# Performance work log

Hardware: AMD Instinct MI355X
Metric: run time of the kernel (lower is better)

Reference implementation:

```python
import jax, jax.numpy as jnp
import numpy as np

H = 25  # fixed state size per module source
N_STEPS = 10


def _lstm_cell(x, h, c, W_ih, W_hh, b_ih, b_hh):
    # PyTorch LSTMCell: gates ordered i, f, g, o
    gates = x @ W_ih.T + b_ih + h @ W_hh.T + b_hh  # [B, 4H]
    i, f, g, o = jnp.split(gates, 4, axis=-1)
    c_new = jax.nn.sigmoid(f) * c + jax.nn.sigmoid(i) * jnp.tanh(g)
    h_new = jax.nn.sigmoid(o) * jnp.tanh(c_new)
    return h_new, c_new


def setup_inputs() -> dict:
    key = jax.random.key(0)
    ks = jax.random.split(key, 11)
    B, A = 131072, 18

    def u(k, shape, fan_in, fan_out):
        bound = np.sqrt(6.0 / (fan_in + fan_out)).astype(np.float32)
        return jax.random.uniform(k, shape, jnp.float32, -bound, bound)

    state = jax.random.normal(ks[0], (B, H), jnp.float32)
    # LSTMCell weights [4H, H]; biases zeroed per module init
    W_ih_enc = u(ks[1], (4 * H, H), H, 4 * H)
    W_hh_enc = u(ks[2], (4 * H, H), H, 4 * H)
    b_ih_enc = jnp.zeros((4 * H,), jnp.float32)
    b_hh_enc = jnp.zeros((4 * H,), jnp.float32)
    W_ih_dec = u(ks[3], (4 * H, H), H, 4 * H)
    W_hh_dec = u(ks[4], (4 * H, H), H, 4 * H)
    b_ih_dec = jnp.zeros((4 * H,), jnp.float32)
    b_hh_dec = jnp.zeros((4 * H,), jnp.float32)
    # actor head: norm_col_init std=0.01, bias 0
    w = jax.random.normal(ks[5], (A, H), jnp.float32)
    W_act = w * (0.01 / jnp.sqrt((w ** 2).sum(1, keepdims=True)))
    b_act = jnp.zeros((A,), jnp.float32)
    return {
        "state_repr_input": state,
        "W_ih_enc": W_ih_enc, "W_hh_enc": W_hh_enc, "b_ih_enc": b_ih_enc, "b_hh_enc": b_hh_enc,
        "W_ih_dec": W_ih_dec, "W_hh_dec": W_hh_dec, "b_ih_dec": b_ih_dec, "b_hh_dec": b_hh_dec,
        "W_act": W_act, "b_act": b_act,
    }


def reference(state_repr_input, W_ih_enc, W_hh_enc, b_ih_enc, b_hh_enc,
              W_ih_dec, W_hh_dec, b_ih_dec, b_hh_dec, W_act, b_act):
    B = state_repr_input.shape[0]
    zeros = jnp.zeros_like(state_repr_input)

    # Encoder: input to each step is previous hx (first step: state)
    def enc_step(carry, _):
        inp, h, c = carry
        h, c = _lstm_cell(inp, h, c, W_ih_enc, W_hh_enc, b_ih_enc, b_hh_enc)
        return (h, h, c), h

    (_, _, _), enc_hs = jax.lax.scan(enc_step, (state_repr_input, zeros, zeros), None, length=N_STEPS)
    # enc_hs: [10, B, 25]

    # Decoder: consumes encoder outputs in order
    def dec_step(carry, x):
        h, c = carry
        h, c = _lstm_cell(x, h, c, W_ih_dec, W_hh_dec, b_ih_dec, b_hh_dec)
        return (h, c), None

    (hx_dec, _), _ = jax.lax.scan(dec_step, (zeros, zeros), enc_hs)

    actor_lang = hx_dec @ W_act.T + b_act  # [B, A]
    return actor_lang, enc_hs
```

## Files before the change

### kernel.cpp

```cpp
#include <hip/hip_runtime.h>


#define HH 25
#define NSTEP 10
#define AOUT 18
#define WPB 4
#define BLK (WPB * 64)
#define NFRG 26
#define FPAD 40
#define LOG2E 1.44269504088896340736f

typedef __attribute__((ext_vector_type(8))) short short8;
typedef __attribute__((ext_vector_type(4))) float f32x4;

__device__ __forceinline__ short f2bf(float x) {
    unsigned u = __float_as_uint(x);
    u += 0x7fffu + ((u >> 16) & 1u);
    return (short)(u >> 16);
}
__device__ __forceinline__ unsigned cvtpk(float lo, float hi) {
    unsigned r;
    asm("v_cvt_pk_bf16_f32 %0, %1, %2" : "=v"(r) : "v"(lo), "v"(hi));
    return r;
}
#if __has_builtin(__builtin_amdgcn_exp2f)
#define EXP2(x) __builtin_amdgcn_exp2f(x)
#else
#define EXP2(x) exp2f(x)
#endif
#define RCP(x) __builtin_amdgcn_rcpf(x)
#define MFMA16(a, b, c) __builtin_amdgcn_mfma_f32_16x16x32_bf16((a), (b), (c), 0, 0, 0)

#define ACT_ELEM(A0, A1, A2, A3, CREF, HOUT)                                   \
    {                                                                          \
        float Ei = EXP2(A0);                                                   \
        float Ef = EXP2(A1);                                                   \
        float Eg = EXP2(A2);                                                   \
        float Eo = EXP2(A3);                                                   \
        float Pf = 1.f + Ef;                                                   \
        float Pig = (1.f + Ei) * (1.f + Eg);                                   \
        float c = fmaf(CREF, Pig, (Eg - 1.f) * Pf) * RCP(Pf * Pig);            \
        CREF = c;                                                              \
        float Ec = EXP2(2.f * LOG2E * c);                                      \
        float Pc = 1.f + Ec;                                                   \
        HOUT = (Pc - 2.f) * RCP(Pc * (1.f + Eo));                              \
    }

__global__ __launch_bounds__(BLK, 4)
void langnn_mfma16(const float* __restrict__ state,
                   const float* __restrict__ Wih_e, const float* __restrict__ Whh_e,
                   const float* __restrict__ bih_e, const float* __restrict__ bhh_e,
                   const float* __restrict__ Wih_d, const float* __restrict__ Whh_d,
                   const float* __restrict__ bih_d, const float* __restrict__ bhh_d,
                   const float* __restrict__ Wact, const float* __restrict__ bact,
                   float* __restrict__ out, int B)
{
    __shared__ __align__(16) short sFrag[NFRG][64][8];
    __shared__ __align__(16) short sH[2][WPB][16][FPAD];

    const int tid  = threadIdx.x;
    const int lane = tid & 63;
    const int w    = tid >> 6;
    const int r    = lane & 15;
    const int g    = lane >> 4;

    for (int i = tid; i < NFRG * 64; i += BLK) {
        const int idx = i >> 6, l = i & 63;
        const int lj = l & 15, lg = l >> 4;
        const float *W1 = nullptr, *W2 = nullptr, *B1 = nullptr, *B2 = nullptr;
        int gt = 0, jt, jmax = HH;
        if (idx < 8)       { gt = idx >> 1;        jt = idx & 1; W1 = Wih_e; W2 = Whh_e; B1 = bih_e; B2 = bhh_e; }
        else if (idx < 16) { gt = (idx - 8) >> 1;  jt = idx & 1; W1 = Wih_d; B1 = bih_d; B2 = bhh_d; }
        else if (idx < 24) { gt = (idx - 16) >> 1; jt = idx & 1; W1 = Whh_d; }
        else               { jt = idx - 24;        W1 = Wact;    B1 = bact;  jmax = AOUT; }
        const bool actor = (idx >= 24);
        const float sc = actor ? 1.f : (gt == 2 ? 2.f * LOG2E : -LOG2E);
        const int col = jt * 16 + lj;
        const int nrow = actor ? col : gt * HH + col;
        for (int e = 0; e < 8; ++e) {
            const int k = lg * 8 + e;
            float v = 0.f;
            if (col < jmax) {
                if (k < HH) {
                    v = W1[nrow * HH + k];
                    if (W2) v += W2[nrow * HH + k];
                    v *= sc;
                } else if (k == HH && B1) {
                    v = B1[nrow];
                    if (B2) v += B2[nrow];
                    v *= sc;
                }
            }
            sFrag[idx][l][e] = f2bf(v);
        }
    }
    {
        int* z = (int*)sH;
        for (int i = tid; i < 2 * WPB * 16 * (FPAD / 2); i += BLK)
            z[i] = ((i % (FPAD / 2)) == 12) ? 0x3F800000 : 0;
    }
    __syncthreads();

    const int b0 = (blockIdx.x * WPB + w) * 16;
    float* pe = out + (size_t)B * AOUT + (size_t)(b0 + g * 4) * HH + r;

    float ce[2][4], cd[2][4];
    #pragma unroll
    for (int jt = 0; jt < 2; ++jt)
        #pragma unroll
        for (int q = 0; q < 4; ++q) { ce[jt][q] = 0.f; cd[jt][q] = 0.f; }

    short8 aE, aD;
    {
        const float* sp0 = state + (size_t)(b0 + r) * HH;
        #pragma unroll
        for (int e = 0; e < 8; ++e) {
            const int k = g * 8 + e;
            aE[e] = (k < HH) ? f2bf(sp0[k]) : (k == HH ? (short)0x3F80 : (short)0);
            aD[e] = (k == HH) ? (short)0x3F80 : (short)0;
        }
    }

    {
        short8 W0f[8];
        #pragma unroll
        for (int gt = 0; gt < 4; ++gt) {
            const float sc = (gt == 2 ? 2.f * LOG2E : -LOG2E);
            #pragma unroll
            for (int jt = 0; jt < 2; ++jt) {
                const int col = jt * 16 + r;
                short8 v8;
                #pragma unroll
                for (int e = 0; e < 8; ++e) {
                    const int k = g * 8 + e;
                    float v = 0.f;
                    if (col < HH) {
                        if (k < HH)       v = Wih_e[(gt * HH + col) * HH + k] * sc;
                        else if (k == HH) v = (bih_e[gt * HH + col] + bhh_e[gt * HH + col]) * sc;
                    }
                    v8[e] = f2bf(v);
                }
                W0f[gt * 2 + jt] = v8;
            }
        }
        #pragma unroll
        for (int jt = 0; jt < 2; ++jt) {
            f32x4 acc[4];
            #pragma unroll
            for (int gt = 0; gt < 4; ++gt) {
                f32x4 z; z[0] = z[1] = z[2] = z[3] = 0.f;
                acc[gt] = MFMA16(aE, W0f[gt * 2 + jt], z);
            }
            float hv[4];
            #pragma unroll
            for (int q = 0; q < 4; ++q)
                ACT_ELEM(acc[0][q], acc[1][q], acc[2][q], acc[3][q], ce[jt][q], hv[q]);
            if (jt == 0 || r < 9) {
                float* p = pe + jt * 16;
                p[0] = hv[0]; p[HH] = hv[1]; p[2 * HH] = hv[2]; p[3 * HH] = hv[3];
                unsigned p01 = cvtpk(hv[0], hv[1]), p23 = cvtpk(hv[2], hv[3]);
                short* sp = &sH[0][w][g * 4][jt * 16 + r];
                sp[0]        = (short)p01;
                sp[FPAD]     = (short)(p01 >> 16);
                sp[2 * FPAD] = (short)p23;
                sp[3 * FPAD] = (short)(p23 >> 16);
            }
        }
        aE = *(const short8*)&sH[0][w][r][g * 8];
        pe += (size_t)B * HH;
    }

    #pragma unroll 1
    for (int t = 0; t < NSTEP - 1; ++t) {
        #pragma unroll
        for (int jt = 0; jt < 2; ++jt) {
            f32x4 accD[4], accE[4];
            #pragma unroll
            for (int gt = 0; gt < 4; ++gt) {
                short8 Bx = *(const short8*)&sFrag[8 + gt * 2 + jt][lane][0];
                short8 Bh = *(const short8*)&sFrag[16 + gt * 2 + jt][lane][0];
                short8 Be = *(const short8*)&sFrag[gt * 2 + jt][lane][0];
                f32x4 z; z[0] = z[1] = z[2] = z[3] = 0.f;
                accD[gt] = MFMA16(aD, Bh, MFMA16(aE, Bx, z));
                accE[gt] = MFMA16(aE, Be, z);
            }
            float hvD[4], hvE[4];
            #pragma unroll
            for (int q = 0; q < 4; ++q) {
                ACT_ELEM(accD[0][q], accD[1][q], accD[2][q], accD[3][q], cd[jt][q], hvD[q]);
                ACT_ELEM(accE[0][q], accE[1][q], accE[2][q], accE[3][q], ce[jt][q], hvE[q]);
            }
            if (jt == 0 || r < 9) {
                float* p = pe + jt * 16;
                p[0] = hvE[0]; p[HH] = hvE[1]; p[2 * HH] = hvE[2]; p[3 * HH] = hvE[3];
                unsigned d01 = cvtpk(hvD[0], hvD[1]), d23 = cvtpk(hvD[2], hvD[3]);
                unsigned e01 = cvtpk(hvE[0], hvE[1]), e23 = cvtpk(hvE[2], hvE[3]);
                short* spD = &sH[1][w][g * 4][jt * 16 + r];
                short* spE = &sH[0][w][g * 4][jt * 16 + r];
                spD[0]        = (short)d01;
                spD[FPAD]     = (short)(d01 >> 16);
                spD[2 * FPAD] = (short)d23;
                spD[3 * FPAD] = (short)(d23 >> 16);
                spE[0]        = (short)e01;
                spE[FPAD]     = (short)(e01 >> 16);
                spE[2 * FPAD] = (short)e23;
                spE[3 * FPAD] = (short)(e23 >> 16);
            }
        }
        aE = *(const short8*)&sH[0][w][r][g * 8];
        aD = *(const short8*)&sH[1][w][r][g * 8];
        pe += (size_t)B * HH;
    }

    #pragma unroll
    for (int jt = 0; jt < 2; ++jt) {
        f32x4 acc[4];
        #pragma unroll
        for (int gt = 0; gt < 4; ++gt) {
            short8 Bx = *(const short8*)&sFrag[8 + gt * 2 + jt][lane][0];
            short8 Bh = *(const short8*)&sFrag[16 + gt * 2 + jt][lane][0];
            f32x4 z; z[0] = z[1] = z[2] = z[3] = 0.f;
            acc[gt] = MFMA16(aD, Bh, MFMA16(aE, Bx, z));
        }
        float hv[4];
        #pragma unroll
        for (int q = 0; q < 4; ++q)
            ACT_ELEM(acc[0][q], acc[1][q], acc[2][q], acc[3][q], cd[jt][q], hv[q]);
        if (jt == 0 || r < 9) {
            unsigned p01 = cvtpk(hv[0], hv[1]), p23 = cvtpk(hv[2], hv[3]);
            short* sp = &sH[1][w][g * 4][jt * 16 + r];
            sp[0]        = (short)p01;
            sp[FPAD]     = (short)(p01 >> 16);
            sp[2 * FPAD] = (short)p23;
            sp[3 * FPAD] = (short)(p23 >> 16);
        }
    }
    aD = *(const short8*)&sH[1][w][r][g * 8];

    #pragma unroll
    for (int jt = 0; jt < 2; ++jt) {
        short8 Bf = *(const short8*)&sFrag[24 + jt][lane][0];
        f32x4 z; z[0] = z[1] = z[2] = z[3] = 0.f;
        f32x4 o = MFMA16(aD, Bf, z);
        if (jt == 0 || r < 2) {
            float* p = out + (size_t)(b0 + g * 4) * AOUT + jt * 16 + r;
            p[0] = o[0]; p[AOUT] = o[1]; p[2 * AOUT] = o[2]; p[3 * AOUT] = o[3];
        }
    }
}

extern "C" void kernel_launch(void* const* d_in, const int* in_sizes, int n_in,
                              void* d_out, int out_size, void* d_ws, size_t ws_size,
                              hipStream_t stream) {
    const float* state = (const float*)d_in[0];
    const float* Wih_e = (const float*)d_in[1];
    const float* Whh_e = (const float*)d_in[2];
    const float* bih_e = (const float*)d_in[3];
    const float* bhh_e = (const float*)d_in[4];
    const float* Wih_d = (const float*)d_in[5];
    const float* Whh_d = (const float*)d_in[6];
    const float* bih_d = (const float*)d_in[7];
    const float* bhh_d = (const float*)d_in[8];
    const float* Wact  = (const float*)d_in[9];
    const float* bact  = (const float*)d_in[10];

    int B = in_sizes[0] / HH;
    int grid = B / (WPB * 16);

    hipLaunchKernelGGL(langnn_mfma16, dim3(grid), dim3(BLK), 0, stream,
                       state, Wih_e, Whh_e, bih_e, bhh_e,
                       Wih_d, Whh_d, bih_d, bhh_d, Wact, bact,
                       (float*)d_out, B);
}
```

Baseline: 115.1 us.

## Swap MFMA operands so hidden state stays in registers, dropping LDS round-trip

Result: faster. 110.1 us (-4.4%).

```diff
diff --git a/kernel.cpp b/kernel.cpp
--- a/kernel.cpp
+++ b/kernel.cpp
@@ -7,11 +7,11 @@
 #define WPB 4
 #define BLK (WPB * 64)
 #define NFRG 26
-#define FPAD 40
 #define LOG2E 1.44269504088896340736f
 
 typedef __attribute__((ext_vector_type(8))) short short8;
 typedef __attribute__((ext_vector_type(4))) float f32x4;
+typedef __attribute__((ext_vector_type(4))) unsigned u32x4;
 
 __device__ __forceinline__ short f2bf(float x) {
     unsigned u = __float_as_uint(x);
@@ -19,9 +19,9 @@
     return (short)(u >> 16);
 }
 __device__ __forceinline__ unsigned cvtpk(float lo, float hi) {
-    unsigned r;
-    asm("v_cvt_pk_bf16_f32 %0, %1, %2" : "=v"(r) : "v"(lo), "v"(hi));
-    return r;
+    unsigned rr;
+    asm("v_cvt_pk_bf16_f32 %0, %1, %2" : "=v"(rr) : "v"(lo), "v"(hi));
+    return rr;
 }
 #if __has_builtin(__builtin_amdgcn_exp2f)
 #define EXP2(x) __builtin_amdgcn_exp2f(x)
@@ -47,16 +47,15 @@
     }
 
 __global__ __launch_bounds__(BLK, 4)
-void langnn_mfma16(const float* __restrict__ state,
-                   const float* __restrict__ Wih_e, const float* __restrict__ Whh_e,
-                   const float* __restrict__ bih_e, const float* __restrict__ bhh_e,
-                   const float* __restrict__ Wih_d, const float* __restrict__ Whh_d,
-                   const float* __restrict__ bih_d, const float* __restrict__ bhh_d,
-                   const float* __restrict__ Wact, const float* __restrict__ bact,
-                   float* __restrict__ out, int B)
+void langnn_swap(const float* __restrict__ state,
+                 const float* __restrict__ Wih_e, const float* __restrict__ Whh_e,
+                 const float* __restrict__ bih_e, const float* __restrict__ bhh_e,
+                 const float* __restrict__ Wih_d, const float* __restrict__ Whh_d,
+                 const float* __restrict__ bih_d, const float* __restrict__ bhh_d,
+                 const float* __restrict__ Wact, const float* __restrict__ bact,
+                 float* __restrict__ out, int B)
 {
     __shared__ __align__(16) short sFrag[NFRG][64][8];
-    __shared__ __align__(16) short sH[2][WPB][16][FPAD];
 
     const int tid  = threadIdx.x;
     const int lane = tid & 63;
@@ -68,24 +67,24 @@
         const int idx = i >> 6, l = i & 63;
         const int lj = l & 15, lg = l >> 4;
         const float *W1 = nullptr, *W2 = nullptr, *B1 = nullptr, *B2 = nullptr;
-        int gt = 0, jt, jmax = HH;
-        if (idx < 8)       { gt = idx >> 1;        jt = idx & 1; W1 = Wih_e; W2 = Whh_e; B1 = bih_e; B2 = bhh_e; }
-        else if (idx < 16) { gt = (idx - 8) >> 1;  jt = idx & 1; W1 = Wih_d; B1 = bih_d; B2 = bhh_d; }
-        else if (idx < 24) { gt = (idx - 16) >> 1; jt = idx & 1; W1 = Whh_d; }
-        else               { jt = idx - 24;        W1 = Wact;    B1 = bact;  jmax = AOUT; }
+        int gt = 0, hf, rmax = HH;
+        if (idx < 8)       { gt = idx >> 1;        hf = idx & 1; W1 = Wih_e; W2 = Whh_e; B1 = bih_e; B2 = bhh_e; }
+        else if (idx < 16) { gt = (idx - 8) >> 1;  hf = idx & 1; W1 = Wih_d; B1 = bih_d; B2 = bhh_d; }
+        else if (idx < 24) { gt = (idx - 16) >> 1; hf = idx & 1; W1 = Whh_d; }
+        else               { hf = idx - 24;        W1 = Wact;    B1 = bact;  rmax = AOUT; }
         const bool actor = (idx >= 24);
         const float sc = actor ? 1.f : (gt == 2 ? 2.f * LOG2E : -LOG2E);
-        const int col = jt * 16 + lj;
-        const int nrow = actor ? col : gt * HH + col;
+        const int row  = hf * 16 + lj;
+        const int nrow = actor ? row : gt * HH + row;
         for (int e = 0; e < 8; ++e) {
-            const int k = lg * 8 + e;
+            const int k = (e < 4) ? lg * 4 + e : 16 + lg * 4 + (e - 4);
             float v = 0.f;
-            if (col < jmax) {
+            if (row < rmax) {
                 if (k < HH) {
                     v = W1[nrow * HH + k];
                     if (W2) v += W2[nrow * HH + k];
                     v *= sc;
-                } else if (k == HH && B1) {
+                } else if (k == 31 && B1) {
                     v = B1[nrow];
                     if (B2) v += B2[nrow];
                     v *= sc;
@@ -94,158 +93,126 @@
             sFrag[idx][l][e] = f2bf(v);
         }
     }
-    {
-        int* z = (int*)sH;
-        for (int i = tid; i < 2 * WPB * 16 * (FPAD / 2); i += BLK)
-            z[i] = ((i % (FPAD / 2)) == 12) ? 0x3F800000 : 0;
-    }
     __syncthreads();
 
     const int b0 = (blockIdx.x * WPB + w) * 16;
-    float* pe = out + (size_t)B * AOUT + (size_t)(b0 + g * 4) * HH + r;
+    float* encBase = out + (size_t)B * AOUT + (size_t)(b0 + r) * HH;
 
     float ce[2][4], cd[2][4];
     #pragma unroll
-    for (int jt = 0; jt < 2; ++jt)
-        #pragma unroll
-        for (int q = 0; q < 4; ++q) { ce[jt][q] = 0.f; cd[jt][q] = 0.f; }
-
-    short8 aE, aD;
+    for (int hf = 0; hf < 2; ++hf)
+        #pragma unroll
+        for (int q = 0; q < 4; ++q) { ce[hf][q] = 0.f; cd[hf][q] = 0.f; }
+
+    short8 hE, hD;
     {
-        const float* sp0 = state + (size_t)(b0 + r) * HH;
+        const float* sp = state + (size_t)(b0 + r) * HH;
         #pragma unroll
         for (int e = 0; e < 8; ++e) {
-            const int k = g * 8 + e;
-            aE[e] = (k < HH) ? f2bf(sp0[k]) : (k == HH ? (short)0x3F80 : (short)0);
-            aD[e] = (k == HH) ? (short)0x3F80 : (short)0;
-        }
-    }
-
-    {
-        short8 W0f[8];
-        #pragma unroll
-        for (int gt = 0; gt < 4; ++gt) {
-            const float sc = (gt == 2 ? 2.f * LOG2E : -LOG2E);
-            #pragma unroll
-            for (int jt = 0; jt < 2; ++jt) {
-                const int col = jt * 16 + r;
-                short8 v8;
-                #pragma unroll
-                for (int e = 0; e < 8; ++e) {
-                    const int k = g * 8 + e;
-                    float v = 0.f;
-                    if (col < HH) {
-                        if (k < HH)       v = Wih_e[(gt * HH + col) * HH + k] * sc;
-                        else if (k == HH) v = (bih_e[gt * HH + col] + bhh_e[gt * HH + col]) * sc;
-                    }
-                    v8[e] = f2bf(v);
-                }
-                W0f[gt * 2 + jt] = v8;
-            }
-        }
-        #pragma unroll
-        for (int jt = 0; jt < 2; ++jt) {
-            f32x4 acc[4];
-            #pragma unroll
-            for (int gt = 0; gt < 4; ++gt) {
-                f32x4 z; z[0] = z[1] = z[2] = z[3] = 0.f;
-                acc[gt] = MFMA16(aE, W0f[gt * 2 + jt], z);
-            }
-            float hv[4];
+            const int k = (e < 4) ? g * 4 + e : 16 + g * 4 + (e - 4);
+            hE[e] = (k < HH) ? f2bf(sp[k]) : (k == 31 ? (short)0x3F80 : (short)0);
+            hD[e] = (k == 31) ? (short)0x3F80 : (short)0;
+        }
+    }
+
+    auto actCell = [&](f32x4 (&acc)[8], float (&cc)[2][4], float (&hv)[2][4]) {
+        #pragma unroll
+        for (int hf = 0; hf < 2; ++hf)
             #pragma unroll
             for (int q = 0; q < 4; ++q)
-                ACT_ELEM(acc[0][q], acc[1][q], acc[2][q], acc[3][q], ce[jt][q], hv[q]);
-            if (jt == 0 || r < 9) {
-                float* p = pe + jt * 16;
-                p[0] = hv[0]; p[HH] = hv[1]; p[2 * HH] = hv[2]; p[3 * HH] = hv[3];
-                unsigned p01 = cvtpk(hv[0], hv[1]), p23 = cvtpk(hv[2], hv[3]);
-                short* sp = &sH[0][w][g * 4][jt * 16 + r];
-                sp[0]        = (short)p01;
-                sp[FPAD]     = (short)(p01 >> 16);
-                sp[2 * FPAD] = (short)p23;
-                sp[3 * FPAD] = (short)(p23 >> 16);
+                ACT_ELEM(acc[0 + hf][q], acc[2 + hf][q], acc[4 + hf][q], acc[6 + hf][q],
+                         cc[hf][q], hv[hf][q]);
+    };
+    auto packH = [&](float (&hv)[2][4]) -> short8 {
+        union { u32x4 d; short8 s; } u;
+        u.d[0] = cvtpk(hv[0][0], hv[0][1]);
+        u.d[1] = cvtpk(hv[0][2], hv[0][3]);
+        u.d[2] = cvtpk(hv[1][0], hv[1][1]);
+        u.d[3] = cvtpk(hv[1][2], (g == 3) ? 1.0f : hv[1][3]);
+        return u.s;
+    };
+    auto storeEnc = [&](int t, float (&hv)[2][4]) {
+        float* p = encBase + (size_t)t * B * HH;
+        #pragma unroll
+        for (int q = 0; q < 4; ++q) p[g * 4 + q] = hv[0][q];
+        #pragma unroll
+        for (int q = 0; q < 4; ++q)
+            if (g * 4 + q < 9) p[16 + g * 4 + q] = hv[1][q];
+    };
+
+    {
+        f32x4 acc[8];
+        #pragma unroll
+        for (int idx = 0; idx < 8; ++idx) {
+            const int gt = idx >> 1, hf = idx & 1;
+            const float sc = (gt == 2) ? 2.f * LOG2E : -LOG2E;
+            const int row = hf * 16 + r;
+            short8 Wf;
+            #pragma unroll
+            for (int e = 0; e < 8; ++e) {
+                const int k = (e < 4) ? g * 4 + e : 16 + g * 4 + (e - 4);
+                float v = 0.f;
+                if (row < HH) {
+                    if (k < HH)       v = Wih_e[(gt * HH + row) * HH + k] * sc;
+                    else if (k == 31) v = (bih_e[gt * HH + row] + bhh_e[gt * HH + row]) * sc;
+                }
+                Wf[e] = f2bf(v);
             }
-        }
-        aE = *(const short8*)&sH[0][w][r][g * 8];
-        pe += (size_t)B * HH;
-    }
+            f32x4 z; z[0] = z[1] = z[2] = z[3] = 0.f;
+            acc[idx] = MFMA16(Wf, hE, z);
+        }
+        float hv[2][4];
+        actCell(acc, ce, hv);
+        storeEnc(0, hv);
+        hE = packH(hv);
+    }
+
+    auto decCell = [&]() {
+        f32x4 acc[8];
+        #pragma unroll
+        for (int idx = 0; idx < 8; ++idx) {
+            short8 Wx = *(const short8*)&sFrag[8 + idx][lane][0];
+            short8 Wh = *(const short8*)&sFrag[16 + idx][lane][0];
+            f32x4 z; z[0] = z[1] = z[2] = z[3] = 0.f;
+            acc[idx] = MFMA16(Wh, hD, MFMA16(Wx, hE, z));
+        }
+        float hv[2][4];
+        actCell(acc, cd, hv);
+        hD = packH(hv);
+    };
+    auto encCell = [&](int t) {
+        f32x4 acc[8];
+        #pragma unroll
+        for (int idx = 0; idx < 8; ++idx) {
+            short8 Wf = *(const short8*)&sFrag[idx][lane][0];
+            f32x4 z; z[0] = z[1] = z[2] = z[3] = 0.f;
+            acc[idx] = MFMA16(Wf, hE, z);
+        }
+        float hv[2][4];
+        actCell(acc, ce, hv);
+        storeEnc(t, hv);
+        hE = packH(hv);
+    };
 
     #pragma unroll 1
     for (int t = 0; t < NSTEP - 1; ++t) {
-        #pragma unroll
-        for (int jt = 0; jt < 2; ++jt) {
-            f32x4 accD[4], accE[4];
-            #pragma unroll
-            for (int gt = 0; gt < 4; ++gt) {
-                short8 Bx = *(const short8*)&sFrag[8 + gt * 2 + jt][lane][0];
-                short8 Bh = *(const short8*)&sFrag[16 + gt * 2 + jt][lane][0];
-                short8 Be = *(const short8*)&sFrag[gt * 2 + jt][lane][0];
-                f32x4 z; z[0] = z[1] = z[2] = z[3] = 0.f;
-                accD[gt] = MFMA16(aD, Bh, MFMA16(aE, Bx, z));
-                accE[gt] = MFMA16(aE, Be, z);
-            }
-            float hvD[4], hvE[4];
-            #pragma unroll
-            for (int q = 0; q < 4; ++q) {
-                ACT_ELEM(accD[0][q], accD[1][q], accD[2][q], accD[3][q], cd[jt][q], hvD[q]);
-                ACT_ELEM(accE[0][q], accE[1][q], accE[2][q], accE[3][q], ce[jt][q], hvE[q]);
-            }
-            if (jt == 0 || r < 9) {
-                float* p = pe + jt * 16;
-                p[0] = hvE[0]; p[HH] = hvE[1]; p[2 * HH] = hvE[2]; p[3 * HH] = hvE[3];
-                unsigned d01 = cvtpk(hvD[0], hvD[1]), d23 = cvtpk(hvD[2], hvD[3]);
-                unsigned e01 = cvtpk(hvE[0], hvE[1]), e23 = cvtpk(hvE[2], hvE[3]);
-                short* spD = &sH[1][w][g * 4][jt * 16 + r];
-                short* spE = &sH[0][w][g * 4][jt * 16 + r];
-                spD[0]        = (short)d01;
-                spD[FPAD]     = (short)(d01 >> 16);
-                spD[2 * FPAD] = (short)d23;
-                spD[3 * FPAD] = (short)(d23 >> 16);
-                spE[0]        = (short)e01;
-                spE[FPAD]     = (short)(e01 >> 16);
-                spE[2 * FPAD] = (short)e23;
-                spE[3 * FPAD] = (short)(e23 >> 16);
-            }
-        }
-        aE = *(const short8*)&sH[0][w][r][g * 8];
-        aD = *(const short8*)&sH[1][w][r][g * 8];
-        pe += (size_t)B * HH;
-    }
-
-    #pragma unroll
-    for (int jt = 0; jt < 2; ++jt) {
-        f32x4 acc[4];
-        #pragma unroll
-        for (int gt = 0; gt < 4; ++gt) {
-            short8 Bx = *(const short8*)&sFrag[8 + gt * 2 + jt][lane][0];
-            short8 Bh = *(const short8*)&sFrag[16 + gt * 2 + jt][lane][0];
-            f32x4 z; z[0] = z[1] = z[2] = z[3] = 0.f;
-            acc[gt] = MFMA16(aD, Bh, MFMA16(aE, Bx, z));
-        }
-        float hv[4];
+        decCell();
+        encCell(t + 1);
+    }
+    decCell();
+
+    {
+        short8 W0 = *(const short8*)&sFrag[24][lane][0];
+        short8 W1 = *(const short8*)&sFrag[25][lane][0];
+        f32x4 z; z[0] = z[1] = z[2] = z[3] = 0.f;
+        f32x4 a0 = MFMA16(W0, hD, z);
+        f32x4 a1 = MFMA16(W1, hD, z);
+        float* p = out + (size_t)(b0 + r) * AOUT;
+        #pragma unroll
+        for (int q = 0; q < 4; ++q) p[g * 4 + q] = a0[q];
         #pragma unroll
         for (int q = 0; q < 4; ++q)
-            ACT_ELEM(acc[0][q], acc[1][q], acc[2][q], acc[3][q], cd[jt][q], hv[q]);
-        if (jt == 0 || r < 9) {
-            unsigned p01 = cvtpk(hv[0], hv[1]), p23 = cvtpk(hv[2], hv[3]);
-            short* sp = &sH[1][w][g * 4][jt * 16 + r];
-            sp[0]        = (short)p01;
-            sp[FPAD]     = (short)(p01 >> 16);
-            sp[2 * FPAD] = (short)p23;
-            sp[3 * FPAD] = (short)(p23 >> 16);
-        }
-    }
-    aD = *(const short8*)&sH[1][w][r][g * 8];
-
-    #pragma unroll
-    for (int jt = 0; jt < 2; ++jt) {
-        short8 Bf = *(const short8*)&sFrag[24 + jt][lane][0];
-        f32x4 z; z[0] = z[1] = z[2] = z[3] = 0.f;
-        f32x4 o = MFMA16(aD, Bf, z);
-        if (jt == 0 || r < 2) {
-            float* p = out + (size_t)(b0 + g * 4) * AOUT + jt * 16 + r;
-            p[0] = o[0]; p[AOUT] = o[1]; p[2 * AOUT] = o[2]; p[3 * AOUT] = o[3];
-        }
+            if (16 + g * 4 + q < AOUT) p[16 + g * 4 + q] = a1[q];
     }
 }
 
@@ -267,7 +234,7 @@
     int B = in_sizes[0] / HH;
     int grid = B / (WPB * 16);
 
-    hipLaunchKernelGGL(langnn_mfma16, dim3(grid), dim3(BLK), 0, stream,
+    hipLaunchKernelGGL(langnn_swap, dim3(grid), dim3(BLK), 0, stream,
                        state, Wih_e, Whh_e, bih_e, bhh_e,
                        Wih_d, Whh_d, bih_d, bhh_d, Wact, bact,
                        (float*)d_out, B);
```

## Warp-specialize encoder and decoder waves with block barriers and two M-tiles

Applied to the files above, without the earlier changes.

New measurement: 107.0 us. 7.0% less time.

```diff
diff --git a/kernel.cpp b/kernel.cpp
--- a/kernel.cpp
+++ b/kernel.cpp
@@ -4,10 +4,11 @@
 #define HH 25
 #define NSTEP 10
 #define AOUT 18
-#define WPB 4
-#define BLK (WPB * 64)
-#define NFRG 26
-#define FPAD 40
+#define BLK 512
+#define NWENC 4
+#define MT 2
+#define NFRG 24
+#define FPAD 32
 #define LOG2E 1.44269504088896340736f
 
 typedef __attribute__((ext_vector_type(8))) short short8;
@@ -19,9 +20,9 @@
     return (short)(u >> 16);
 }
 __device__ __forceinline__ unsigned cvtpk(float lo, float hi) {
-    unsigned r;
-    asm("v_cvt_pk_bf16_f32 %0, %1, %2" : "=v"(r) : "v"(lo), "v"(hi));
-    return r;
+    unsigned rr;
+    asm("v_cvt_pk_bf16_f32 %0, %1, %2" : "=v"(rr) : "v"(lo), "v"(hi));
+    return rr;
 }
 #if __has_builtin(__builtin_amdgcn_exp2f)
 #define EXP2(x) __builtin_amdgcn_exp2f(x)
@@ -47,16 +48,17 @@
     }
 
 __global__ __launch_bounds__(BLK, 4)
-void langnn_mfma16(const float* __restrict__ state,
-                   const float* __restrict__ Wih_e, const float* __restrict__ Whh_e,
-                   const float* __restrict__ bih_e, const float* __restrict__ bhh_e,
-                   const float* __restrict__ Wih_d, const float* __restrict__ Whh_d,
-                   const float* __restrict__ bih_d, const float* __restrict__ bhh_d,
-                   const float* __restrict__ Wact, const float* __restrict__ bact,
-                   float* __restrict__ out, int B)
+void langnn_ws(const float* __restrict__ state,
+               const float* __restrict__ Wih_e, const float* __restrict__ Whh_e,
+               const float* __restrict__ bih_e, const float* __restrict__ bhh_e,
+               const float* __restrict__ Wih_d, const float* __restrict__ Whh_d,
+               const float* __restrict__ bih_d, const float* __restrict__ bhh_d,
+               const float* __restrict__ Wact, const float* __restrict__ bact,
+               float* __restrict__ out, int B)
 {
     __shared__ __align__(16) short sFrag[NFRG][64][8];
-    __shared__ __align__(16) short sH[2][WPB][16][FPAD];
+    __shared__ __align__(16) short sHE[2][128][FPAD];
+    __shared__ __align__(16) short sHD[NWENC][32][FPAD];
 
     const int tid  = threadIdx.x;
     const int lane = tid & 63;
@@ -68,19 +70,17 @@
         const int idx = i >> 6, l = i & 63;
         const int lj = l & 15, lg = l >> 4;
         const float *W1 = nullptr, *W2 = nullptr, *B1 = nullptr, *B2 = nullptr;
-        int gt = 0, jt, jmax = HH;
+        int gt, jt;
         if (idx < 8)       { gt = idx >> 1;        jt = idx & 1; W1 = Wih_e; W2 = Whh_e; B1 = bih_e; B2 = bhh_e; }
         else if (idx < 16) { gt = (idx - 8) >> 1;  jt = idx & 1; W1 = Wih_d; B1 = bih_d; B2 = bhh_d; }
-        else if (idx < 24) { gt = (idx - 16) >> 1; jt = idx & 1; W1 = Whh_d; }
-        else               { jt = idx - 24;        W1 = Wact;    B1 = bact;  jmax = AOUT; }
-        const bool actor = (idx >= 24);
-        const float sc = actor ? 1.f : (gt == 2 ? 2.f * LOG2E : -LOG2E);
+        else               { gt = (idx - 16) >> 1; jt = idx & 1; W1 = Whh_d; }
+        const float sc = (gt == 2 ? 2.f * LOG2E : -LOG2E);
         const int col = jt * 16 + lj;
-        const int nrow = actor ? col : gt * HH + col;
+        const int nrow = gt * HH + col;
         for (int e = 0; e < 8; ++e) {
             const int k = lg * 8 + e;
             float v = 0.f;
-            if (col < jmax) {
+            if (col < HH) {
                 if (k < HH) {
                     v = W1[nrow * HH + k];
                     if (W2) v += W2[nrow * HH + k];
@@ -95,41 +95,58 @@
         }
     }
     {
-        int* z = (int*)sH;
-        for (int i = tid; i < 2 * WPB * 16 * (FPAD / 2); i += BLK)
-            z[i] = ((i % (FPAD / 2)) == 12) ? 0x3F800000 : 0;
+        int* zE = (int*)sHE;
+        for (int i = tid; i < 2 * 128 * (FPAD / 2); i += BLK)
+            zE[i] = ((i % (FPAD / 2)) == 12) ? 0x3F800000 : 0;
+        int* zD = (int*)sHD;
+        for (int i = tid; i < NWENC * 32 * (FPAD / 2); i += BLK)
+            zD[i] = ((i % (FPAD / 2)) == 12) ? 0x3F800000 : 0;
     }
     __syncthreads();
 
-    const int b0 = (blockIdx.x * WPB + w) * 16;
-    float* pe = out + (size_t)B * AOUT + (size_t)(b0 + g * 4) * HH + r;
-
-    float ce[2][4], cd[2][4];
+    const bool isEnc = (w < NWENC);
+    const int wl = isEnc ? w : (w - NWENC);
+    const int rowBase = wl * 32;
+    const int gBase = blockIdx.x * 128 + rowBase;
+
+    float cc[MT][2][4];
     #pragma unroll
-    for (int jt = 0; jt < 2; ++jt)
-        #pragma unroll
-        for (int q = 0; q < 4; ++q) { ce[jt][q] = 0.f; cd[jt][q] = 0.f; }
-
-    short8 aE, aD;
-    {
-        const float* sp0 = state + (size_t)(b0 + r) * HH;
+    for (int mt = 0; mt < MT; ++mt)
+        #pragma unroll
+        for (int jt = 0; jt < 2; ++jt)
+            #pragma unroll
+            for (int q = 0; q < 4; ++q) cc[mt][jt][q] = 0.f;
+
+    short8 aE[MT], aD[MT];
+    #pragma unroll
+    for (int mt = 0; mt < MT; ++mt) {
         #pragma unroll
         for (int e = 0; e < 8; ++e) {
             const int k = g * 8 + e;
-            aE[e] = (k < HH) ? f2bf(sp0[k]) : (k == HH ? (short)0x3F80 : (short)0);
-            aD[e] = (k == HH) ? (short)0x3F80 : (short)0;
-        }
-    }
-
-    {
-        short8 W0f[8];
-        #pragma unroll
-        for (int gt = 0; gt < 4; ++gt) {
-            const float sc = (gt == 2 ? 2.f * LOG2E : -LOG2E);
-            #pragma unroll
-            for (int jt = 0; jt < 2; ++jt) {
+            aD[mt][e] = (k == HH) ? (short)0x3F80 : (short)0;
+        }
+    }
+    if (isEnc) {
+        #pragma unroll
+        for (int mt = 0; mt < MT; ++mt) {
+            const float* sp0 = state + (size_t)(gBase + mt * 16 + r) * HH;
+            #pragma unroll
+            for (int e = 0; e < 8; ++e) {
+                const int k = g * 8 + e;
+                aE[mt][e] = (k < HH) ? f2bf(sp0[k]) : (k == HH ? (short)0x3F80 : (short)0);
+            }
+        }
+    }
+
+    if (isEnc) {
+        #pragma unroll
+        for (int jt = 0; jt < 2; ++jt) {
+            f32x4 acc[MT][4];
+            #pragma unroll
+            for (int gt = 0; gt < 4; ++gt) {
+                const float sc = (gt == 2) ? 2.f * LOG2E : -LOG2E;
                 const int col = jt * 16 + r;
-                short8 v8;
+                short8 Wf;
                 #pragma unroll
                 for (int e = 0; e < 8; ++e) {
                     const int k = g * 8 + e;
@@ -138,113 +155,178 @@
                         if (k < HH)       v = Wih_e[(gt * HH + col) * HH + k] * sc;
                         else if (k == HH) v = (bih_e[gt * HH + col] + bhh_e[gt * HH + col]) * sc;
                     }
-                    v8[e] = f2bf(v);
-                }
-                W0f[gt * 2 + jt] = v8;
-            }
-        }
+                    Wf[e] = f2bf(v);
+                }
+                f32x4 z; z[0] = z[1] = z[2] = z[3] = 0.f;
+                #pragma unroll
+                for (int mt = 0; mt < MT; ++mt) acc[mt][gt] = MFMA16(aE[mt], Wf, z);
+            }
+            #pragma unroll
+            for (int mt = 0; mt < MT; ++mt) {
+                float hv[4];
+                #pragma unroll
+                for (int q = 0; q < 4; ++q)
+                    ACT_ELEM(acc[mt][0][q], acc[mt][1][q], acc[mt][2][q], acc[mt][3][q],
+                             cc[mt][jt][q], hv[q]);
+                if (jt == 0 || r < 9) {
+                    float* p = out + (size_t)B * AOUT
+                             + (size_t)(gBase + mt * 16 + g * 4) * HH + jt * 16 + r;
+                    p[0] = hv[0]; p[HH] = hv[1]; p[2 * HH] = hv[2]; p[3 * HH] = hv[3];
+                    unsigned p01 = cvtpk(hv[0], hv[1]), p23 = cvtpk(hv[2], hv[3]);
+                    short* sp = &sHE[0][rowBase + mt * 16 + g * 4][jt * 16 + r];
+                    sp[0]        = (short)p01;
+                    sp[FPAD]     = (short)(p01 >> 16);
+                    sp[2 * FPAD] = (short)p23;
+                    sp[3 * FPAD] = (short)(p23 >> 16);
+                }
+            }
+        }
+        #pragma unroll
+        for (int mt = 0; mt < MT; ++mt)
+            aE[mt] = *(const short8*)&sHE[0][rowBase + mt * 16 + r][g * 8];
+    }
+    __syncthreads();
+
+    #pragma unroll 1
+    for (int t = 1; t < NSTEP; ++t) {
+        if (isEnc) {
+            const int buf = t & 1;
+            #pragma unroll
+            for (int jt = 0; jt < 2; ++jt) {
+                f32x4 acc[MT][4];
+                #pragma unroll
+                for (int gt = 0; gt < 4; ++gt) {
+                    short8 Bf = *(const short8*)&sFrag[gt * 2 + jt][lane][0];
+                    f32x4 z; z[0] = z[1] = z[2] = z[3] = 0.f;
+                    #pragma unroll
+                    for (int mt = 0; mt < MT; ++mt) acc[mt][gt] = MFMA16(aE[mt], Bf, z);
+                }
+                #pragma unroll
+                for (int mt = 0; mt < MT; ++mt) {
+                    float hv[4];
+                    #pragma unroll
+                    for (int q = 0; q < 4; ++q)
+                        ACT_ELEM(acc[mt][0][q], acc[mt][1][q], acc[mt][2][q], acc[mt][3][q],
+                                 cc[mt][jt][q], hv[q]);
+                    if (jt == 0 || r < 9) {
+                        float* p = out + (size_t)B * AOUT + (size_t)t * B * HH
+                                 + (size_t)(gBase + mt * 16 + g * 4) * HH + jt * 16 + r;
+                        p[0] = hv[0]; p[HH] = hv[1]; p[2 * HH] = hv[2]; p[3 * HH] = hv[3];
+                        unsigned p01 = cvtpk(hv[0], hv[1]), p23 = cvtpk(hv[2], hv[3]);
+                        short* sp = &sHE[buf][rowBase + mt * 16 + g * 4][jt * 16 + r];
+                        sp[0]        = (short)p01;
+                        sp[FPAD]     = (short)(p01 >> 16);
+                        sp[2 * FPAD] = (short)p23;
+                        sp[3 * FPAD] = (short)(p23 >> 16);
+                    }
+                }
+            }
+            #pragma unroll
+            for (int mt = 0; mt < MT; ++mt)
+                aE[mt] = *(const short8*)&sHE[buf][rowBase + mt * 16 + r][g * 8];
+        } else {
+            const int buf = (t - 1) & 1;
+            short8 aEd[MT];
+            #pragma unroll
+            for (int mt = 0; mt < MT; ++mt)
+                aEd[mt] = *(const short8*)&sHE[buf][rowBase + mt * 16 + r][g * 8];
+            #pragma unroll
+            for (int jt = 0; jt < 2; ++jt) {
+                f32x4 acc[MT][4];
+                #pragma unroll
+                for (int gt = 0; gt < 4; ++gt) {
+                    short8 Bx = *(const short8*)&sFrag[8 + gt * 2 + jt][lane][0];
+                    short8 Bh = *(const short8*)&sFrag[16 + gt * 2 + jt][lane][0];
+                    f32x4 z; z[0] = z[1] = z[2] = z[3] = 0.f;
+                    #pragma unroll
+                    for (int mt = 0; mt < MT; ++mt)
+                        acc[mt][gt] = MFMA16(aD[mt], Bh, MFMA16(aEd[mt], Bx, z));
+                }
+                #pragma unroll
+                for (int mt = 0; mt < MT; ++mt) {
+                    float hv[4];
+                    #pragma unroll
+                    for (int q = 0; q < 4; ++q)
+                        ACT_ELEM(acc[mt][0][q], acc[mt][1][q], acc[mt][2][q], acc[mt][3][q],
+                                 cc[mt][jt][q], hv[q]);
+                    if (jt == 0 || r < 9) {
+                        unsigned p01 = cvtpk(hv[0], hv[1]), p23 = cvtpk(hv[2], hv[3]);
+                        short* sp = &sHD[wl][mt * 16 + g * 4][jt * 16 + r];
+                        sp[0]        = (short)p01;
+                        sp[FPAD]     = (short)(p01 >> 16);
+                        sp[2 * FPAD] = (short)p23;
+                        sp[3 * FPAD] = (short)(p23 >> 16);
+                    }
+                }
+            }
+            #pragma unroll
+            for (int mt = 0; mt < MT; ++mt)
+                aD[mt] = *(const short8*)&sHD[wl][mt * 16 + r][g * 8];
+        }
+        __syncthreads();
+    }
+
+    if (!isEnc) {
+        short8 aEd[MT];
+        #pragma unroll
+        for (int mt = 0; mt < MT; ++mt)
+            aEd[mt] = *(const short8*)&sHE[(NSTEP - 1) & 1][rowBase + mt * 16 + r][g * 8];
         #pragma unroll
         for (int jt = 0; jt < 2; ++jt) {
-            f32x4 acc[4];
-            #pragma unroll
-            for (int gt = 0; gt < 4; ++gt) {
-                f32x4 z; z[0] = z[1] = z[2] = z[3] = 0.f;
-                acc[gt] = MFMA16(aE, W0f[gt * 2 + jt], z);
-            }
-            float hv[4];
-            #pragma unroll
-            for (int q = 0; q < 4; ++q)
-                ACT_ELEM(acc[0][q], acc[1][q], acc[2][q], acc[3][q], ce[jt][q], hv[q]);
-            if (jt == 0 || r < 9) {
-                float* p = pe + jt * 16;
-                p[0] = hv[0]; p[HH] = hv[1]; p[2 * HH] = hv[2]; p[3 * HH] = hv[3];
-                unsigned p01 = cvtpk(hv[0], hv[1]), p23 = cvtpk(hv[2], hv[3]);
-                short* sp = &sH[0][w][g * 4][jt * 16 + r];
-                sp[0]        = (short)p01;
-                sp[FPAD]     = (short)(p01 >> 16);
-                sp[2 * FPAD] = (short)p23;
-                sp[3 * FPAD] = (short)(p23 >> 16);
-            }
-        }
-        aE = *(const short8*)&sH[0][w][r][g * 8];
-        pe += (size_t)B * HH;
-    }
-
-    #pragma unroll 1
-    for (int t = 0; t < NSTEP - 1; ++t) {
-        #pragma unroll
-        for (int jt = 0; jt < 2; ++jt) {
-            f32x4 accD[4], accE[4];
+            f32x4 acc[MT][4];
             #pragma unroll
             for (int gt = 0; gt < 4; ++gt) {
                 short8 Bx = *(const short8*)&sFrag[8 + gt * 2 + jt][lane][0];
                 short8 Bh = *(const short8*)&sFrag[16 + gt * 2 + jt][lane][0];
-                short8 Be = *(const short8*)&sFrag[gt * 2 + jt][lane][0];
                 f32x4 z; z[0] = z[1] = z[2] = z[3] = 0.f;
-                accD[gt] = MFMA16(aD, Bh, MFMA16(aE, Bx, z));
-                accE[gt] = MFMA16(aE, Be, z);
-            }
-            float hvD[4], hvE[4];
-            #pragma unroll
-            for (int q = 0; q < 4; ++q) {
-                ACT_ELEM(accD[0][q], accD[1][q], accD[2][q], accD[3][q], cd[jt][q], hvD[q]);
-                ACT_ELEM(accE[0][q], accE[1][q], accE[2][q], accE[3][q], ce[jt][q], hvE[q]);
-            }
-            if (jt == 0 || r < 9) {
-                float* p = pe + jt * 16;
-                p[0] = hvE[0]; p[HH] = hvE[1]; p[2 * HH] = hvE[2]; p[3 * HH] = hvE[3];
-                unsigned d01 = cvtpk(hvD[0], hvD[1]), d23 = cvtpk(hvD[2], hvD[3]);
-                unsigned e01 = cvtpk(hvE[0], hvE[1]), e23 = cvtpk(hvE[2], hvE[3]);
-                short* spD = &sH[1][w][g * 4][jt * 16 + r];
-                short* spE = &sH[0][w][g * 4][jt * 16 + r];
-                spD[0]        = (short)d01;
-                spD[FPAD]     = (short)(d01 >> 16);
-                spD[2 * FPAD] = (short)d23;
-                spD[3 * FPAD] = (short)(d23 >> 16);
-                spE[0]        = (short)e01;
-                spE[FPAD]     = (short)(e01 >> 16);
-                spE[2 * FPAD] = (short)e23;
-                spE[3 * FPAD] = (short)(e23 >> 16);
-            }
-        }
-        aE = *(const short8*)&sH[0][w][r][g * 8];
-        aD = *(const short8*)&sH[1][w][r][g * 8];
-        pe += (size_t)B * HH;
-    }
-
-    #pragma unroll
-    for (int jt = 0; jt < 2; ++jt) {
-        f32x4 acc[4];
-        #pragma unroll
-        for (int gt = 0; gt < 4; ++gt) {
-            short8 Bx = *(const short8*)&sFrag[8 + gt * 2 + jt][lane][0];
-            short8 Bh = *(const short8*)&sFrag[16 + gt * 2 + jt][lane][0];
+                #pragma unroll
+                for (int mt = 0; mt < MT; ++mt)
+                    acc[mt][gt] = MFMA16(aD[mt], Bh, MFMA16(aEd[mt], Bx, z));
+            }
+            #pragma unroll
+            for (int mt = 0; mt < MT; ++mt) {
+                float hv[4];
+                #pragma unroll
+                for (int q = 0; q < 4; ++q)
+                    ACT_ELEM(acc[mt][0][q], acc[mt][1][q], acc[mt][2][q], acc[mt][3][q],
+                             cc[mt][jt][q], hv[q]);
+                if (jt == 0 || r < 9) {
+                    unsigned p01 = cvtpk(hv[0], hv[1]), p23 = cvtpk(hv[2], hv[3]);
+                    short* sp = &sHD[wl][mt * 16 + g * 4][jt * 16 + r];
+                    sp[0]        = (short)p01;
+                    sp[FPAD]     = (short)(p01 >> 16);
+                    sp[2 * FPAD] = (short)p23;
+                    sp[3 * FPAD] = (short)(p23 >> 16);
+                }
+            }
+        }
+        #pragma unroll
+        for (int mt = 0; mt < MT; ++mt)
+            aD[mt] = *(const short8*)&sHD[wl][mt * 16 + r][g * 8];
+
+        #pragma unroll
+        for (int jt = 0; jt < 2; ++jt) {
+            const int col = jt * 16 + r;
+            short8 Bf;
+            #pragma unroll
+            for (int e = 0; e < 8; ++e) {
+                const int k = g * 8 + e;
+                float v = 0.f;
+                if (col < AOUT) {
+                    if (k < HH)       v = Wact[col * HH + k];
+                    else if (k == HH) v = bact[col];
+                }
+                Bf[e] = f2bf(v);
+            }
             f32x4 z; z[0] = z[1] = z[2] = z[3] = 0.f;
-            acc[gt] = MFMA16(aD, Bh, MFMA16(aE, Bx, z));
-        }
-        float hv[4];
-        #pragma unroll
-        for (int q = 0; q < 4; ++q)
-            ACT_ELEM(acc[0][q], acc[1][q], acc[2][q], acc[3][q], cd[jt][q], hv[q]);
-        if (jt == 0 || r < 9) {
-            unsigned p01 = cvtpk(hv[0], hv[1]), p23 = cvtpk(hv[2], hv[3]);
-            short* sp = &sH[1][w][g * 4][jt * 16 + r];
-            sp[0]        = (short)p01;
-            sp[FPAD]     = (short)(p01 >> 16);
-            sp[2 * FPAD] = (short)p23;
-            sp[3 * FPAD] = (short)(p23 >> 16);
-        }
-    }
-    aD = *(const short8*)&sH[1][w][r][g * 8];
-
-    #pragma unroll
-    for (int jt = 0; jt < 2; ++jt) {
-        short8 Bf = *(const short8*)&sFrag[24 + jt][lane][0];
-        f32x4 z; z[0] = z[1] = z[2] = z[3] = 0.f;
-        f32x4 o = MFMA16(aD, Bf, z);
-        if (jt == 0 || r < 2) {
-            float* p = out + (size_t)(b0 + g * 4) * AOUT + jt * 16 + r;
-            p[0] = o[0]; p[AOUT] = o[1]; p[2 * AOUT] = o[2]; p[3 * AOUT] = o[3];
+            #pragma unroll
+            for (int mt = 0; mt < MT; ++mt) {
+                f32x4 o = MFMA16(aD[mt], Bf, z);
+                if (jt == 0 || r < 2) {
+                    float* p = out + (size_t)(gBase + mt * 16 + g * 4) * AOUT + jt * 16 + r;
+                    p[0] = o[0]; p[AOUT] = o[1]; p[2 * AOUT] = o[2]; p[3 * AOUT] = o[3];
+                }
+            }
         }
     }
 }
@@ -265,9 +347,9 @@
     const float* bact  = (const float*)d_in[10];
 
     int B = in_sizes[0] / HH;
-    int grid = B / (WPB * 16);
-
-    hipLaunchKernelGGL(langnn_mfma16, dim3(grid), dim3(BLK), 0, stream,
+    int grid = B / 128;
+
+    hipLaunchKernelGGL(langnn_ws, dim3(grid), dim3(BLK), 0, stream,
                        state, Wih_e, Whh_e, bih_e, bhh_e,
                        Wih_d, Whh_d, bih_d, bhh_d, Wact, bact,
                        (float*)d_out, B);
```
